# Kernel optimization log

Hardware: AMD Instinct MI355X
Metric: run time of the kernel (lower is better)

The kernel has to match this reference:

```python
import jax, jax.numpy as jnp
import numpy as np
from jax import lax

B, T, F_IN = 8, 512, 229
C1 = 48            # model_size_conv // 16
C3 = 96            # model_size_conv // 8
D_CONV = 768       # model_size_conv
D_LSTM = 768       # model_size_lstm
N_PITCH = 88       # MAX_MIDI - MIN_MIDI + 1
N_STATE = 5
EMB = 2
LSTM_IN = D_CONV + N_PITCH * EMB   # 944
FC_IN = C3 * (F_IN // 4)           # 96 * 57 = 5472
BN_EPS = 1e-5


def setup_inputs() -> dict:
    key = jax.random.key(0)
    ks = iter(jax.random.split(key, 64))
    nrm = lambda shape, s=0.05: jax.random.normal(next(ks), shape, jnp.float32) * s
    uni = lambda shape: jax.random.uniform(next(ks), shape, jnp.float32, 0.5, 1.5)
    inp = {
        'mel': jax.random.normal(next(ks), (B, T, F_IN), jnp.float32),
        'conv1_w': nrm((C1, 1, 3, 3)), 'conv1_b': nrm((C1,)),
        'bn1_g': uni((C1,)), 'bn1_b': nrm((C1,)), 'bn1_m': nrm((C1,), 0.1), 'bn1_v': uni((C1,)),
        'conv2_w': nrm((C1, C1, 3, 3)), 'conv2_b': nrm((C1,)),
        'bn2_g': uni((C1,)), 'bn2_b': nrm((C1,)), 'bn2_m': nrm((C1,), 0.1), 'bn2_v': uni((C1,)),
        'conv3_w': nrm((C3, C1, 3, 3)), 'conv3_b': nrm((C3,)),
        'bn3_g': uni((C3,)), 'bn3_b': nrm((C3,)), 'bn3_m': nrm((C3,), 0.1), 'bn3_v': uni((C3,)),
        'fc_w': nrm((D_CONV, FC_IN)), 'fc_b': nrm((D_CONV,)),
        'wih1': nrm((4 * D_LSTM, LSTM_IN)), 'whh1': nrm((4 * D_LSTM, D_LSTM)),
        'bih1': nrm((4 * D_LSTM,)), 'bhh1': nrm((4 * D_LSTM,)),
        'wih2': nrm((4 * D_LSTM, D_LSTM)), 'whh2': nrm((4 * D_LSTM, D_LSTM)),
        'bih2': nrm((4 * D_LSTM,)), 'bhh2': nrm((4 * D_LSTM,)),
        'post_w': nrm((N_PITCH * N_STATE, D_LSTM)), 'post_b': nrm((N_PITCH * N_STATE,)),
        'emb_w': nrm((N_STATE, EMB), 1.0),
    }
    return inp


def _conv_bn_relu(x, w, b, g, be, m, v):
    # x: NCHW, w: OIHW, padding 'SAME' == padding=1 for 3x3
    y = lax.conv_general_dilated(x, w, (1, 1), 'SAME', dimension_numbers=('NCHW', 'OIHW', 'NCHW'))
    y = y + b[None, :, None, None]
    scale = (g / jnp.sqrt(v + BN_EPS))[None, :, None, None]
    y = (y - m[None, :, None, None]) * scale + be[None, :, None, None]
    return jax.nn.relu(y)


def _maxpool12(x):
    # MaxPool2d((1,2)) on NCHW, floor mode
    return lax.reduce_window(x, -jnp.inf, lax.max, (1, 1, 1, 2), (1, 1, 1, 2), 'VALID')


def _lstm_cell(x, h, c, wih, whh, bih, bhh):
    z = x @ wih.T + h @ whh.T + bih + bhh
    i, f, g, o = jnp.split(z, 4, axis=-1)
    c = jax.nn.sigmoid(f) * c + jax.nn.sigmoid(i) * jnp.tanh(g)
    h = jax.nn.sigmoid(o) * jnp.tanh(c)
    return h, c


def _forward(mel, conv1_w, conv1_b, bn1_g, bn1_b, bn1_m, bn1_v,
             conv2_w, conv2_b, bn2_g, bn2_b, bn2_m, bn2_v,
             conv3_w, conv3_b, bn3_g, bn3_b, bn3_m, bn3_v,
             fc_w, fc_b, wih1, whh1, bih1, bhh1, wih2, whh2, bih2, bhh2,
             post_w, post_b, emb_w):
    b = mel.shape[0]
    # --- ConvStack acoustic model (eval mode: dropout = identity) ---
    x = mel[:, None]                                  # (B,1,T,F)
    x = _conv_bn_relu(x, conv1_w, conv1_b, bn1_g, bn1_b, bn1_m, bn1_v)
    x = _conv_bn_relu(x, conv2_w, conv2_b, bn2_g, bn2_b, bn2_m, bn2_v)
    x = _maxpool12(x)
    x = _conv_bn_relu(x, conv3_w, conv3_b, bn3_g, bn3_b, bn3_m, bn3_v)
    x = _maxpool12(x)                                 # (B,C3,T,F//4)
    x = x.transpose(0, 2, 1, 3).reshape(b, -1, FC_IN) # (B,T,C3*F//4)
    acoustic = x @ fc_w.T + fc_b                      # (B,T,768)

    def step(carry, a_t):
        h1, c1, h2, c2, prev = carry                  # prev: (B,88) int32
        emb = emb_w[prev].reshape(prev.shape[0], N_PITCH * EMB)
        xt = jnp.concatenate([a_t, emb], axis=-1)     # (B,944)
        h1n, c1n = _lstm_cell(xt, h1, c1, wih1, whh1, bih1, bhh1)
        h2n, c2n = _lstm_cell(h1n, h2, c2, wih2, whh2, bih2, bhh2)
        logits = (h2n @ post_w.T + post_b).reshape(-1, N_PITCH, N_STATE)
        nprev = jnp.argmax(logits, axis=-1).astype(jnp.int32)  # argmax(softmax)==argmax(logits)
        return (h1n, c1n, h2n, c2n, nprev), logits

    z = jnp.zeros((b, D_LSTM), mel.dtype)
    prev0 = jnp.zeros((b, N_PITCH), jnp.int32)
    _, logits = lax.scan(step, (z, z, z, z, prev0), acoustic.transpose(1, 0, 2))
    return logits.transpose(1, 0, 2, 3)               # (B,T,88,N_STATE)


def reference(mel, conv1_w, conv1_b, bn1_g, bn1_b, bn1_m, bn1_v,
              conv2_w, conv2_b, bn2_g, bn2_b, bn2_m, bn2_v,
              conv3_w, conv3_b, bn3_g, bn3_b, bn3_m, bn3_v,
              fc_w, fc_b, wih1, whh1, bih1, bhh1, wih2, whh2, bih2, bhh2,
              post_w, post_b, emb_w):
    return _forward(mel, conv1_w, conv1_b, bn1_g, bn1_b, bn1_m, bn1_v,
                    conv2_w, conv2_b, bn2_g, bn2_b, bn2_m, bn2_v,
                    conv3_w, conv3_b, bn3_g, bn3_b, bn3_m, bn3_v,
                    fc_w, fc_b, wih1, whh1, bih1, bhh1, wih2, whh2, bih2, bhh2,
                    post_w, post_b, emb_w)
```

## Files before the change

### kernel.cpp

```cpp
#include <hip/hip_runtime.h>
#include <math.h>

#define WS_C3   0u
#define WS_C2CH 22413312u
#define WS_AC   28104192u
#define WS_A1   0u

__device__ __forceinline__ float sigm(float x){ return 1.0f / (1.0f + expf(-x)); }

__device__ __forceinline__ void cstore(float* p, float v){
  union { float f; unsigned u; } c; c.f = v;
  __hip_atomic_store((unsigned*)p, c.u, __ATOMIC_RELAXED,
                     __HIP_MEMORY_SCOPE_SYSTEM);
}
__device__ __forceinline__ void cload64(const float* p, float& a, float& b){
  unsigned long long u = __hip_atomic_load((const unsigned long long*)p,
                          __ATOMIC_RELAXED, __HIP_MEMORY_SCOPE_SYSTEM);
  union { unsigned long long u; float f[2]; } c; c.u = u;
  a = c.f[0]; b = c.f[1];
}
__device__ __forceinline__ unsigned cloadu(const unsigned* p){
  return __hip_atomic_load(p, __ATOMIC_RELAXED, __HIP_MEMORY_SCOPE_SYSTEM);
}
__device__ __forceinline__ unsigned long long cloadu64(const void* p){
  return __hip_atomic_load((const unsigned long long*)p, __ATOMIC_RELAXED,
                           __HIP_MEMORY_SCOPE_SYSTEM);
}
__device__ __forceinline__ void cstoreu64(void* p, unsigned long long v){
  __hip_atomic_store((unsigned long long*)p, v, __ATOMIC_RELAXED,
                     __HIP_MEMORY_SCOPE_SYSTEM);
}

#define SLOT 16
#define FLG  4112
__device__ __forceinline__ void gbar(unsigned* sy, unsigned bar, int wg){
  __syncthreads();
  const int tid = threadIdx.x;
  if (tid == 0)
    __hip_atomic_store(&sy[SLOT + wg*16], bar, __ATOMIC_RELAXED,
                       __HIP_MEMORY_SCOPE_SYSTEM);
  if (wg == 255){
    if (tid < 64){
      for (;;){
        unsigned m0 = cloadu(&sy[SLOT + (4*tid + 0)*16]);
        unsigned m1 = cloadu(&sy[SLOT + (4*tid + 1)*16]);
        unsigned m2 = cloadu(&sy[SLOT + (4*tid + 2)*16]);
        unsigned m3 = cloadu(&sy[SLOT + (4*tid + 3)*16]);
        unsigned a = m0 < m1 ? m0 : m1;
        unsigned b = m2 < m3 ? m2 : m3;
        unsigned mn = a < b ? a : b;
        if (__all(mn >= bar)) break;
        __builtin_amdgcn_s_sleep(1);
      }
    }
    __syncthreads();
    __hip_atomic_store(&sy[FLG + tid*16], bar, __ATOMIC_RELAXED,
                       __HIP_MEMORY_SCOPE_SYSTEM);
  } else {
    if (tid == 0){
      while (cloadu(&sy[FLG + wg*16]) < bar)
        __builtin_amdgcn_s_sleep(1);
    }
  }
  __syncthreads();
}

__global__ __launch_bounds__(256) void conv2f_k(
    const float* __restrict__ mel, const float* __restrict__ w1,
    const float* __restrict__ b1, const float* __restrict__ g1,
    const float* __restrict__ be1, const float* __restrict__ m1,
    const float* __restrict__ v1,
    const float* __restrict__ w2, const float* __restrict__ b2,
    const float* __restrict__ g2, const float* __restrict__ be2,
    const float* __restrict__ m2, const float* __restrict__ v2,
    float* __restrict__ c2ch, int t0)
{
  __shared__ float act[3*8*240];
  __shared__ float w2s[48*8*12];
  __shared__ float mel5[5*240];
  __shared__ float w1s[48*12];
  __shared__ float sc1[48], sh1[48], sc2[48], sh2[48];
  int tid = threadIdx.x;
  int b = blockIdx.x / 130, lt = blockIdx.x - b*130;
  int t = t0 - 1 + lt;

  int fg = tid % 29, ocg = tid / 29;
  int f0 = fg * 8, oc0 = ocg * 6;

  if (t < 0 || t > 511){
    if (tid < 232){
      for (int o = 0; o < 6; ++o)
        for (int jj = 0; jj < 4; ++jj){
          int fp = fg*4 + jj;
          if (fp < 114)
            c2ch[((b*48 + oc0 + o)*130 + lt)*114 + fp] = 0.f;
        }
    }
    return;
  }

  for (int idx = tid; idx < 5*240; idx += 256){
    int rr = idx / 240, w = idx - rr*240;
    int tt = t + rr - 2, f = w - 2;
    mel5[idx] = (tt >= 0 && tt < 512 && f >= 0 && f < 229)
                ? mel[(b*512 + tt)*229 + f] : 0.f;
  }
  for (int idx = tid; idx < 48*12; idx += 256){
    int c = idx / 12, q = idx - c*12;
    int kh = q >> 2, kw = q & 3;
    w1s[idx] = (kw < 3) ? w1[c*9 + kh*3 + kw] : 0.f;
  }
  if (tid < 48){
    float s1 = g1[tid] / sqrtf(v1[tid] + 1e-5f);
    sc1[tid] = s1; sh1[tid] = be1[tid] + (b1[tid] - m1[tid]) * s1;
    float s2 = g2[tid] / sqrtf(v2[tid] + 1e-5f);
    sc2[tid] = s2; sh2[tid] = be2[tid] + (b2[tid] - m2[tid]) * s2;
  }

  float acc[6][8];
  #pragma unroll
  for (int o = 0; o < 6; ++o)
    #pragma unroll
    for (int j = 0; j < 8; ++j) acc[o][j] = 0.f;

  for (int ch = 0; ch < 6; ++ch){
    int ci0 = ch * 8;
    __syncthreads();
    for (int idx = tid; idx < 3*8*240; idx += 256){
      int rr = idx / 1920;
      int rem = idx - rr*1920;
      int ci = rem / 240, w = rem - ci*240;
      int tt = t + rr - 1, f = w - 1;
      float val = 0.f;
      if (tt >= 0 && tt < 512 && f >= 0 && f < 229){
        int cg = ci0 + ci;
        float a = 0.f;
        #pragma unroll
        for (int dh = 0; dh < 3; ++dh){
          const float* mr = &mel5[(rr + dh)*240 + w];
          a = fmaf(mr[0], w1s[cg*12 + dh*4 + 0], a);
          a = fmaf(mr[1], w1s[cg*12 + dh*4 + 1], a);
          a = fmaf(mr[2], w1s[cg*12 + dh*4 + 2], a);
        }
        a = a * sc1[cg] + sh1[cg];
        val = a > 0.f ? a : 0.f;
      }
      act[idx] = val;
    }
    for (int idx = tid; idx < 48*8*12; idx += 256){
      int oc = idx / 96;
      int rem = idx - oc*96;
      int ci = rem / 12, q = rem - ci*12;
      int kh = q >> 2, kw = q & 3;
      w2s[idx] = (kw < 3) ? w2[(oc*48 + ci0 + ci)*9 + kh*3 + kw] : 0.f;
    }
    __syncthreads();
    if (tid < 232){
      for (int ci = 0; ci < 8; ++ci){
        #pragma unroll
        for (int kh = 0; kh < 3; ++kh){
          const float* ap = &act[(kh*8 + ci)*240 + f0];
          float4 A0 = *(const float4*)(ap);
          float4 A1v = *(const float4*)(ap + 4);
          float4 A2 = *(const float4*)(ap + 8);
          float L[12] = {A0.x,A0.y,A0.z,A0.w,A1v.x,A1v.y,A1v.z,A1v.w,A2.x,A2.y,A2.z,A2.w};
          #pragma unroll
          for (int o = 0; o < 6; ++o){
            float4 wv = *(const float4*)&w2s[((oc0 + o)*8 + ci)*12 + kh*4];
            #pragma unroll
            for (int j = 0; j < 8; ++j)
              acc[o][j] = fmaf(L[j+2], wv.z, fmaf(L[j+1], wv.y, fmaf(L[j], wv.x, acc[o][j])));
          }
        }
      }
    }
  }
  __syncthreads();
  if (tid < 232){
    #pragma unroll
    for (int o = 0; o < 6; ++o){
      int oc = oc0 + o;
      float s = sc2[oc], hs = sh2[oc];
      #pragma unroll
      for (int jj = 0; jj < 4; ++jj){
        int fp = fg*4 + jj;
        if (fp < 114){
          float v0 = acc[o][2*jj] * s + hs;   v0 = v0 > 0.f ? v0 : 0.f;
          float v1 = acc[o][2*jj+1] * s + hs; v1 = v1 > 0.f ? v1 : 0.f;
          c2ch[((b*48 + oc)*130 + lt)*114 + fp] = v0 > v1 ? v0 : v1;
        }
      }
    }
  }
}

__global__ __launch_bounds__(256) void conv3_k(
    const float* __restrict__ c2ch, const float* __restrict__ w3,
    const float* __restrict__ b3, const float* __restrict__ g3,
    const float* __restrict__ be3, const float* __restrict__ m3,
    const float* __restrict__ v3, float* __restrict__ c3p, int t0)
{
  __shared__ float act[3*8*128];
  __shared__ float w3s[96*8*12];
  __shared__ float sc[96], sh[96];
  int tid = threadIdx.x;
  int b = blockIdx.x >> 7, tl = blockIdx.x & 127;
  int t = t0 + tl;
  if (tid < 96){
    float s = g3[tid] / sqrtf(v3[tid] + 1e-5f);
    sc[tid] = s; sh[tid] = be3[tid] + (b3[tid] - m3[tid]) * s;
  }
  int fg = tid % 15, ocg = tid / 15;
  int f0 = fg * 8, oc0 = ocg * 6;
  float acc[6][8];
  #pragma unroll
  for (int o = 0; o < 6; ++o)
    #pragma unroll
    for (int j = 0; j < 8; ++j) acc[o][j] = 0.f;

  for (int ch = 0; ch < 6; ++ch){
    int ci0 = ch * 8;
    __syncthreads();
    for (int idx = tid; idx < 3*8*128; idx += 256){
      int rr = idx >> 10;
      int rem = idx & 1023;
      int ci = rem >> 7, w = rem & 127;
      int lt = tl + rr;
      int f = w - 1;
      float val = 0.f;
      if (f >= 0 && f < 114)
        val = c2ch[((b*48 + ci0 + ci)*130 + lt)*114 + f];
      act[idx] = val;
    }
    for (int idx = tid; idx < 96*8*12; idx += 256){
      int oc = idx / 96;
      int rem = idx - oc*96;
      int ci = rem / 12, q = rem - ci*12;
      int kh = q >> 2, kw = q & 3;
      w3s[idx] = (kw < 3) ? w3[(oc*48 + ci0 + ci)*9 + kh*3 + kw] : 0.f;
    }
    __syncthreads();
    if (tid < 240){
      for (int ci = 0; ci < 8; ++ci){
        #pragma unroll
        for (int kh = 0; kh < 3; ++kh){
          const float* ap = &act[(kh*8 + ci)*128 + f0];
          float4 A0 = *(const float4*)(ap);
          float4 A1v = *(const float4*)(ap + 4);
          float4 A2 = *(const float4*)(ap + 8);
          float L[12] = {A0.x,A0.y,A0.z,A0.w,A1v.x,A1v.y,A1v.z,A1v.w,A2.x,A2.y,A2.z,A2.w};
          #pragma unroll
          for (int o = 0; o < 6; ++o){
            float4 wv = *(const float4*)&w3s[((oc0 + o)*8 + ci)*12 + kh*4];
            #pragma unroll
            for (int j = 0; j < 8; ++j)
              acc[o][j] = fmaf(L[j+2], wv.z, fmaf(L[j+1], wv.y, fmaf(L[j], wv.x, acc[o][j])));
          }
        }
      }
    }
  }
  __syncthreads();
  if (tid < 240){
    #pragma unroll
    for (int o = 0; o < 6; ++o){
      int oc = oc0 + o;
      float s = sc[oc], hs = sh[oc];
      #pragma unroll
      for (int jj = 0; jj < 4; ++jj){
        int fp = fg*4 + jj;
        if (fp < 57){
          float v0 = acc[o][2*jj] * s + hs;   v0 = v0 > 0.f ? v0 : 0.f;
          float v1 = acc[o][2*jj+1] * s + hs; v1 = v1 > 0.f ? v1 : 0.f;
          c3p[((b*96 + oc)*512 + t)*57 + fp] = v0 > v1 ? v0 : v1;
        }
      }
    }
  }
}

__global__ __launch_bounds__(256) void gemm_fc_k(
    const float* __restrict__ c3p, const float* __restrict__ fcw,
    const float* __restrict__ fcb, float* __restrict__ ac)
{
  __shared__ float As[16*132];
  __shared__ float Bs[16*132];
  int tid = threadIdx.x;
  int m0 = blockIdx.x * 128, n0 = blockIdx.y * 128;
  int tm = (tid & 15) * 8, tn = (tid >> 4) * 8;
  float acc[8][8];
  #pragma unroll
  for (int i = 0; i < 8; ++i)
    #pragma unroll
    for (int j = 0; j < 8; ++j) acc[i][j] = 0.f;

  for (int k0 = 0; k0 < 5472; k0 += 16){
    __syncthreads();
    #pragma unroll
    for (int i = 0; i < 8; ++i){
      int idx = i*256 + tid;
      int k = idx & 15, mm = idx >> 4;
      int gk = k0 + k;
      int ci = (gk * 36793) >> 21;
      int f  = gk - ci*57;
      int gm = m0 + mm;
      int bb = gm >> 9, tt = gm & 511;
      As[k*132 + mm] = c3p[((bb*96 + ci)*512 + tt)*57 + f];
      Bs[k*132 + mm] = fcw[(n0 + mm)*5472 + gk];
    }
    __syncthreads();
    #pragma unroll
    for (int k = 0; k < 16; ++k){
      const float* arow = &As[k*132 + tm];
      const float* brow = &Bs[k*132 + tn];
      float4 a0 = *(const float4*)arow, a1 = *(const float4*)(arow + 4);
      float4 b0 = *(const float4*)brow, b1 = *(const float4*)(brow + 4);
      float av[8] = {a0.x,a0.y,a0.z,a0.w,a1.x,a1.y,a1.z,a1.w};
      float bv[8] = {b0.x,b0.y,b0.z,b0.w,b1.x,b1.y,b1.z,b1.w};
      #pragma unroll
      for (int i = 0; i < 8; ++i)
        #pragma unroll
        for (int j = 0; j < 8; ++j)
          acc[i][j] = fmaf(av[i], bv[j], acc[i][j]);
    }
  }
  #pragma unroll
  for (int i = 0; i < 8; ++i){
    int gm = m0 + tm + i;
    #pragma unroll
    for (int j = 0; j < 8; ++j){
      int gn = n0 + tn + j;
      ac[gm*768 + gn] = acc[i][j] + fcb[gn];
    }
  }
}

__global__ __launch_bounds__(256) void gemm_a1_k(
    const float* __restrict__ ac, const float* __restrict__ wih1,
    const float* __restrict__ bih1, const float* __restrict__ bhh1,
    float* __restrict__ A1)
{
  __shared__ float As[16*132];
  __shared__ float Bs[16*132];
  int tid = threadIdx.x;
  int m0 = blockIdx.x * 128, n0 = blockIdx.y * 128;
  int tm = (tid & 15) * 8, tn = (tid >> 4) * 8;
  float acc[8][8];
  #pragma unroll
  for (int i = 0; i < 8; ++i)
    #pragma unroll
    for (int j = 0; j < 8; ++j) acc[i][j] = 0.f;

  for (int k0 = 0; k0 < 768; k0 += 16){
    __syncthreads();
    #pragma unroll
    for (int i = 0; i < 8; ++i){
      int idx = i*256 + tid;
      int k = idx & 15, mm = idx >> 4;
      int gk = k0 + k;
      As[k*132 + mm] = ac[(m0 + mm)*768 + gk];
      Bs[k*132 + mm] = wih1[(n0 + mm)*944 + gk];
    }
    __syncthreads();
    #pragma unroll
    for (int k = 0; k < 16; ++k){
      const float* arow = &As[k*132 + tm];
      const float* brow = &Bs[k*132 + tn];
      float4 a0 = *(const float4*)arow, a1 = *(const float4*)(arow + 4);
      float4 b0 = *(const float4*)brow, b1 = *(const float4*)(brow + 4);
      float av[8] = {a0.x,a0.y,a0.z,a0.w,a1.x,a1.y,a1.z,a1.w};
      float bv[8] = {b0.x,b0.y,b0.z,b0.w,b1.x,b1.y,b1.z,b1.w};
      #pragma unroll
      for (int i = 0; i < 8; ++i)
        #pragma unroll
        for (int j = 0; j < 8; ++j)
          acc[i][j] = fmaf(av[i], bv[j], acc[i][j]);
    }
  }
  #pragma unroll
  for (int i = 0; i < 8; ++i){
    int gm = m0 + tm + i;
    int tt = gm & 511, bb = gm >> 9;
    #pragma unroll
    for (int j = 0; j < 8; ++j){
      int gn = n0 + tn + j;
      A1[tt*24576 + gn*8 + bb] = acc[i][j] + bih1[gn] + bhh1[gn];
    }
  }
}

#define S2 772
__global__ __launch_bounds__(256, 1) void rec_k(
    const float* __restrict__ A1,
    const float* __restrict__ whh1, const float* __restrict__ wih1,
    const float* __restrict__ wih2, const float* __restrict__ whh2,
    const float* __restrict__ bih2, const float* __restrict__ bhh2,
    const float* __restrict__ postw, const float* __restrict__ postb,
    const float* __restrict__ embw,
    float* __restrict__ xbuf, float* __restrict__ hbuf,
    unsigned* __restrict__ slt, unsigned* __restrict__ sy,
    float* __restrict__ out)
{
  const int wg = blockIdx.x, tid = threadIdx.x;
  const int wv = tid >> 6, l = tid & 63;
  __shared__ float xs[8*S2];
  __shared__ float h2s[8*S2];
  __shared__ float cvec[88*5*12];
  __shared__ float zbuf[96];
  __shared__ float red2[160];
  __shared__ unsigned smax[88];

  float wA[12][3];
  float wB[24][3];
  float wC[3][5];
  {
    int Rb = wv*768 + wg*3;
    #pragma unroll
    for (int ki = 0; ki < 12; ++ki){
      int k = l + (ki << 6);
      #pragma unroll
      for (int u = 0; u < 3; ++u)
        wA[ki][u] = whh1[(Rb + u)*768 + k];
    }
    #pragma unroll
    for (int ki = 0; ki < 24; ++ki){
      int k = l + (ki << 6);
      #pragma unroll
      for (int u = 0; u < 3; ++u)
        wB[ki][u] = (k < 768) ? wih2[(Rb + u)*768 + k] : whh2[(Rb + u)*768 + k - 768];
    }
  }
  if (wg < 88){
    #pragma unroll
    for (int kc = 0; kc < 3; ++kc)
      #pragma unroll
      for (int s = 0; s < 5; ++s)
        wC[kc][s] = postw[(wg*5 + s)*768 + tid + (kc << 8)];
  }
  float b2r = 0.f; int fR = 0, fb = 0;
  if (tid < 96){
    int g = tid / 24, rem = tid - g*24;
    int u = rem >> 3; fb = rem & 7;
    fR = g*768 + wg*3 + u;
    b2r = bih2[fR] + bhh2[fR];
  }
  float pbr = (wg < 88 && tid < 40) ? postb[wg*5 + (tid >> 3)] : 0.f;
  float c1r = 0.f, c2r = 0.f;

  for (int idx = tid; idx < 88*5*12; idx += 256){
    int p = idx / 60, rem = idx - p*60;
    int s = rem / 12, r = rem - s*12;
    int g = r / 3, u = r - g*3;
    int row = g*768 + wg*3 + u;
    cvec[idx] = wih1[row*944 + 768 + 2*p]     * embw[s*2]
              + wih1[row*944 + 768 + 2*p + 1] * embw[s*2 + 1];
  }
  for (int idx = tid; idx < 8*S2; idx += 256){ h2s[idx] = 0.f; xs[idx] = 0.f; }
  __syncthreads();

  unsigned bar = 0;

  for (int t = 0; t < 512; ++t){
    float* xn = xbuf + (t & 1) * 6144;
    float* hw = hbuf + (t & 1) * 6144;
    const float* hr = hbuf + ((t ^ 1) & 1) * 6144;

    float a1v = 0.f;
    if (tid < 96) a1v = A1[t*24576 + fR*8 + fb];

    float r0[8], r1[8], r2[8];
    #pragma unroll
    for (int q = 0; q < 8; ++q){ r0[q] = 0.f; r1[q] = 0.f; r2[q] = 0.f; }
    if (t > 0){
      #pragma unroll
      for (int q = 0; q < 4; ++q){
        cload64(hr + (tid      )*8 + 2*q, r0[2*q], r0[2*q+1]);
        cload64(hr + (tid + 256)*8 + 2*q, r1[2*q], r1[2*q+1]);
        cload64(hr + (tid + 512)*8 + 2*q, r2[2*q], r2[2*q+1]);
      }
      if (wg < 88){
        float accL[5][8];
        #pragma unroll
        for (int s = 0; s < 5; ++s)
          #pragma unroll
          for (int j = 0; j < 8; ++j)
            accL[s][j] = fmaf(wC[2][s], r2[j],
                         fmaf(wC[1][s], r1[j], wC[0][s]*r0[j]));
        #pragma unroll
        for (int s = 0; s < 5; ++s)
          #pragma unroll
          for (int j = 0; j < 8; ++j){
            float v = accL[s][j];
            v += __shfl_xor(v, 1);  v += __shfl_xor(v, 2);  v += __shfl_xor(v, 4);
            v += __shfl_xor(v, 8);  v += __shfl_xor(v, 16); v += __shfl_xor(v, 32);
            if (l == 0) red2[(s*8 + j)*4 + wv] = v;
          }
        __syncthreads();
        if (tid < 40){
          float sum = red2[tid*4] + red2[tid*4 + 1] + red2[tid*4 + 2] + red2[tid*4 + 3] + pbr;
          int s = tid >> 3, bb = tid & 7;
          out[bb*225280 + (t-1)*440 + wg*5 + s] = sum;
          zbuf[tid] = sum;
        }
        __syncthreads();
        int bs = 0;
        if (tid < 8){
          float best = zbuf[tid];
          #pragma unroll
          for (int s = 1; s < 5; ++s){
            float v = zbuf[s*8 + tid];
            if (v > best){ best = v; bs = s; }
          }
        }
        if (wv == 0){
          unsigned lo = 0;
          #pragma unroll
          for (int b = 0; b < 8; ++b)
            lo |= (unsigned)(__shfl(bs, b) & 7) << (4*b);
          if (l == 0){
            unsigned long long pv =
                ((unsigned long long)(unsigned)t << 32) | (unsigned long long)lo;
            cstoreu64((unsigned long long*)slt + ((size_t)(t & 1)*88 + wg)*8, pv);
          }
        }
      }
    }

    float acc1[3][8];
    #pragma unroll
    for (int u = 0; u < 3; ++u)
      #pragma unroll
      for (int j = 0; j < 8; ++j) acc1[u][j] = 0.f;
    #pragma unroll
    for (int ki = 0; ki < 12; ++ki){
      int k = l + (ki << 6);
      float x0 = xs[k],        x1 = xs[S2 + k],   x2 = xs[2*S2 + k], x3 = xs[3*S2 + k];
      float x4 = xs[4*S2 + k], x5 = xs[5*S2 + k], x6 = xs[6*S2 + k], x7 = xs[7*S2 + k];
      #pragma unroll
      for (int u = 0; u < 3; ++u){
        float w = wA[ki][u];
        acc1[u][0] = fmaf(w, x0, acc1[u][0]);
        acc1[u][1] = fmaf(w, x1, acc1[u][1]);
        acc1[u][2] = fmaf(w, x2, acc1[u][2]);
        acc1[u][3] = fmaf(w, x3, acc1[u][3]);
        acc1[u][4] = fmaf(w, x4, acc1[u][4]);
        acc1[u][5] = fmaf(w, x5, acc1[u][5]);
        acc1[u][6] = fmaf(w, x6, acc1[u][6]);
        acc1[u][7] = fmaf(w, x7, acc1[u][7]);
      }
    }

    __syncthreads();
    #pragma unroll
    for (int p = 0; p < 8; ++p){
      h2s[p*S2 + tid]       = r0[p];
      h2s[p*S2 + tid + 256] = r1[p];
      h2s[p*S2 + tid + 512] = r2[p];
    }
    #pragma unroll
    for (int u = 0; u < 3; ++u)
      #pragma unroll
      for (int j = 0; j < 8; ++j){
        float s = acc1[u][j];
        s += __shfl_xor(s, 1);  s += __shfl_xor(s, 2);  s += __shfl_xor(s, 4);
        s += __shfl_xor(s, 8);  s += __shfl_xor(s, 16); s += __shfl_xor(s, 32);
        if (l == 0) zbuf[wv*24 + u*8 + j] = s;
      }
    if (wv == 0){
      const unsigned long long* sl =
          (const unsigned long long*)slt + (size_t)(t & 1) * 88 * 8;
      unsigned lo0 = 0, lo1 = 0;
      for (;;){
        unsigned long long v0 = cloadu64(&sl[l*8]);
        unsigned long long v1 = 0xffffffffffffffffull;
        if (l < 24) v1 = cloadu64(&sl[(64 + l)*8]);
        unsigned t0v = (unsigned)(v0 >> 32);
        unsigned t1v = (unsigned)(v1 >> 32);
        unsigned mn = t0v < t1v ? t0v : t1v;
        if (__all(mn >= (unsigned)t)){ lo0 = (unsigned)v0; lo1 = (unsigned)v1; break; }
        __builtin_amdgcn_s_sleep(1);
      }
      smax[l] = lo0;
      if (l < 24) smax[64 + l] = lo1;
    }
    __syncthreads();
    if (tid < 96){
      int g = tid / 24;
      int rowidx = g*3 + ((tid - g*24) >> 3);
      int b = tid & 7;
      float z = zbuf[tid] + a1v;
      for (int p = 0; p < 88; ++p){
        int s = (smax[p] >> (b*4)) & 7;
        z += cvec[(p*5 + s)*12 + rowidx];
      }
      zbuf[tid] = z;
    }
    __syncthreads();
    if (tid < 24){
      float zi = zbuf[tid], zf = zbuf[24 + tid], zg = zbuf[48 + tid], zo = zbuf[72 + tid];
      c1r = sigm(zf)*c1r + sigm(zi)*tanhf(zg);
      float hh = sigm(zo)*tanhf(c1r);
      cstore(&xn[wg*24 + tid], hh);
    }
    ++bar; gbar(sy, bar, wg);

    {
      float sa[12], sb[12];
      #pragma unroll
      for (int i = 0; i < 12; ++i){
        int idx = tid + (i << 8);
        cload64(xn + 2*idx, sa[i], sb[i]);
      }
      float acc[3][8];
      #pragma unroll
      for (int u = 0; u < 3; ++u)
        #pragma unroll
        for (int j = 0; j < 8; ++j) acc[u][j] = 0.f;
      #pragma unroll
      for (int ki = 12; ki < 24; ++ki){
        int k = l + ((ki - 12) << 6);
        float x0 = h2s[k],        x1 = h2s[S2 + k],   x2 = h2s[2*S2 + k], x3 = h2s[3*S2 + k];
        float x4 = h2s[4*S2 + k], x5 = h2s[5*S2 + k], x6 = h2s[6*S2 + k], x7 = h2s[7*S2 + k];
        #pragma unroll
        for (int u = 0; u < 3; ++u){
          float w = wB[ki][u];
          acc[u][0] = fmaf(w, x0, acc[u][0]);
          acc[u][1] = fmaf(w, x1, acc[u][1]);
          acc[u][2] = fmaf(w, x2, acc[u][2]);
          acc[u][3] = fmaf(w, x3, acc[u][3]);
          acc[u][4] = fmaf(w, x4, acc[u][4]);
          acc[u][5] = fmaf(w, x5, acc[u][5]);
          acc[u][6] = fmaf(w, x6, acc[u][6]);
          acc[u][7] = fmaf(w, x7, acc[u][7]);
        }
      }
      #pragma unroll
      for (int i = 0; i < 12; ++i){
        int idx = tid + (i << 8);
        int k = idx >> 2, p = (idx & 3) << 1;
        xs[p*S2 + k]       = sa[i];
        xs[(p + 1)*S2 + k] = sb[i];
      }
      __syncthreads();
      #pragma unroll
      for (int ki = 0; ki < 12; ++ki){
        int k = l + (ki << 6);
        float x0 = xs[k],        x1 = xs[S2 + k],   x2 = xs[2*S2 + k], x3 = xs[3*S2 + k];
        float x4 = xs[4*S2 + k], x5 = xs[5*S2 + k], x6 = xs[6*S2 + k], x7 = xs[7*S2 + k];
        #pragma unroll
        for (int u = 0; u < 3; ++u){
          float w = wB[ki][u];
          acc[u][0] = fmaf(w, x0, acc[u][0]);
          acc[u][1] = fmaf(w, x1, acc[u][1]);
          acc[u][2] = fmaf(w, x2, acc[u][2]);
          acc[u][3] = fmaf(w, x3, acc[u][3]);
          acc[u][4] = fmaf(w, x4, acc[u][4]);
          acc[u][5] = fmaf(w, x5, acc[u][5]);
          acc[u][6] = fmaf(w, x6, acc[u][6]);
          acc[u][7] = fmaf(w, x7, acc[u][7]);
        }
      }
      #pragma unroll
      for (int u = 0; u < 3; ++u)
        #pragma unroll
        for (int j = 0; j < 8; ++j){
          float s = acc[u][j];
          s += __shfl_xor(s, 1);  s += __shfl_xor(s, 2);  s += __shfl_xor(s, 4);
          s += __shfl_xor(s, 8);  s += __shfl_xor(s, 16); s += __shfl_xor(s, 32);
          if (l == 0) zbuf[wv*24 + u*8 + j] = s;
        }
      __syncthreads();
      if (tid < 96)
        zbuf[tid] += b2r;
      __syncthreads();
      if (tid < 24){
        float zi = zbuf[tid], zf = zbuf[24 + tid], zg = zbuf[48 + tid], zo = zbuf[72 + tid];
        c2r = sigm(zf)*c2r + sigm(zi)*tanhf(zg);
        float hh = sigm(zo)*tanhf(c2r);
        cstore(&hw[wg*24 + tid], hh);
      }
      ++bar; gbar(sy, bar, wg);
    }
  }

  if (wg < 88){
    const float* hr = hbuf + 6144;
    float r0[8], r1[8], r2[8];
    #pragma unroll
    for (int q = 0; q < 4; ++q){
      cload64(hr + (tid      )*8 + 2*q, r0[2*q], r0[2*q+1]);
      cload64(hr + (tid + 256)*8 + 2*q, r1[2*q], r1[2*q+1]);
      cload64(hr + (tid + 512)*8 + 2*q, r2[2*q], r2[2*q+1]);
    }
    float accL[5][8];
    #pragma unroll
    for (int s = 0; s < 5; ++s)
      #pragma unroll
      for (int j = 0; j < 8; ++j)
        accL[s][j] = fmaf(wC[2][s], r2[j],
                     fmaf(wC[1][s], r1[j], wC[0][s]*r0[j]));
    #pragma unroll
    for (int s = 0; s < 5; ++s)
      #pragma unroll
      for (int j = 0; j < 8; ++j){
        float v = accL[s][j];
        v += __shfl_xor(v, 1);  v += __shfl_xor(v, 2);  v += __shfl_xor(v, 4);
        v += __shfl_xor(v, 8);  v += __shfl_xor(v, 16); v += __shfl_xor(v, 32);
        if (l == 0) red2[(s*8 + j)*4 + wv] = v;
      }
    __syncthreads();
    if (tid < 40){
      float sum = red2[tid*4] + red2[tid*4 + 1] + red2[tid*4 + 2] + red2[tid*4 + 3] + pbr;
      int s = tid >> 3, bb = tid & 7;
      out[bb*225280 + 511*440 + wg*5 + s] = sum;
    }
  }
}

extern "C" void kernel_launch(void* const* d_in, const int* in_sizes, int n_in,
                              void* d_out, int out_size, void* d_ws, size_t ws_size,
                              hipStream_t stream)
{
  (void)in_sizes; (void)n_in; (void)out_size; (void)ws_size;
  const float* mel  = (const float*)d_in[0];
  const float* w1   = (const float*)d_in[1];
  const float* b1   = (const float*)d_in[2];
  const float* g1   = (const float*)d_in[3];
  const float* be1  = (const float*)d_in[4];
  const float* m1   = (const float*)d_in[5];
  const float* v1   = (const float*)d_in[6];
  const float* w2   = (const float*)d_in[7];
  const float* b2   = (const float*)d_in[8];
  const float* g2   = (const float*)d_in[9];
  const float* be2  = (const float*)d_in[10];
  const float* m2   = (const float*)d_in[11];
  const float* v2   = (const float*)d_in[12];
  const float* w3   = (const float*)d_in[13];
  const float* b3   = (const float*)d_in[14];
  const float* g3   = (const float*)d_in[15];
  const float* be3  = (const float*)d_in[16];
  const float* m3   = (const float*)d_in[17];
  const float* v3   = (const float*)d_in[18];
  const float* fcw  = (const float*)d_in[19];
  const float* fcb  = (const float*)d_in[20];
  const float* wih1 = (const float*)d_in[21];
  const float* whh1 = (const float*)d_in[22];
  const float* bih1 = (const float*)d_in[23];
  const float* bhh1 = (const float*)d_in[24];
  const float* wih2 = (const float*)d_in[25];
  const float* whh2 = (const float*)d_in[26];
  const float* bih2 = (const float*)d_in[27];
  const float* bhh2 = (const float*)d_in[28];
  const float* postw= (const float*)d_in[29];
  const float* postb= (const float*)d_in[30];
  const float* embw = (const float*)d_in[31];

  float* ws    = (float*)d_ws;
  float* c3p   = ws + WS_C3;
  float* c2ch  = ws + WS_C2CH;
  float* ac    = ws + WS_AC;
  float* A1    = ws + WS_A1;
  float* st    = ws + WS_AC;
  float* xbuf  = st;
  float* hbuf  = st + 12288;
  unsigned* slt = (unsigned*)(st + 24576);
  unsigned* sy  = (unsigned*)(st + 27392);
  float* outp  = (float*)d_out;

  for (int c = 0; c < 4; ++c){
    int t0 = c * 128;
    conv2f_k<<<dim3(8*130), dim3(256), 0, stream>>>(
        mel, w1, b1, g1, be1, m1, v1, w2, b2, g2, be2, m2, v2, c2ch, t0);
    conv3_k<<<dim3(8*128), dim3(256), 0, stream>>>(
        c2ch, w3, b3, g3, be3, m3, v3, c3p, t0);
  }
  gemm_fc_k<<<dim3(32, 6), dim3(256), 0, stream>>>(c3p, fcw, fcb, ac);
  gemm_a1_k<<<dim3(32, 24), dim3(256), 0, stream>>>(ac, wih1, bih1, bhh1, A1);

  hipMemsetAsync(st, 0, 35600 * sizeof(float), stream);

  rec_k<<<dim3(256), dim3(256), 0, stream>>>(
      A1, whh1, wih1, wih2, whh2, bih2, bhh2, postw, postb, embw,
      xbuf, hbuf, slt, sy, outp);
}
```

Before: 19.06 ms.

## Overlap output projection and argmax with the grid barrier using tagged h2 slots

Splits the grid barrier into arrive and wait phases. The 88 post-projection workgroups now poll tagged 64-bit h2 values (timestep in the high word) and compute logits and argmax for the current step between arrive and wait, instead of after the next barrier. This moves the projection and argmax off the critical path of the next step's input stage. In exchange it adds a second h2 buffer with tag words, per-element spin polling, and a larger workspace memset.

```diff
diff --git a/kernel.cpp b/kernel.cpp
--- a/kernel.cpp
+++ b/kernel.cpp
@@ -30,15 +30,23 @@
   __hip_atomic_store((unsigned long long*)p, v, __ATOMIC_RELAXED,
                      __HIP_MEMORY_SCOPE_SYSTEM);
 }
+__device__ __forceinline__ float u2f(unsigned u){
+  union { unsigned u; float f; } c; c.u = u; return c.f;
+}
+__device__ __forceinline__ unsigned f2u(float f){
+  union { unsigned u; float f; } c; c.f = f; return c.u;
+}
 
 #define SLOT 16
 #define FLG  4112
-__device__ __forceinline__ void gbar(unsigned* sy, unsigned bar, int wg){
+__device__ __forceinline__ void gbar_arrive(unsigned* sy, unsigned bar, int wg){
   __syncthreads();
-  const int tid = threadIdx.x;
-  if (tid == 0)
+  if (threadIdx.x == 0)
     __hip_atomic_store(&sy[SLOT + wg*16], bar, __ATOMIC_RELAXED,
                        __HIP_MEMORY_SCOPE_SYSTEM);
+}
+__device__ __forceinline__ void gbar_wait(unsigned* sy, unsigned bar, int wg){
+  const int tid = threadIdx.x;
   if (wg == 255){
     if (tid < 64){
       for (;;){
@@ -63,6 +71,10 @@
     }
   }
   __syncthreads();
+}
+__device__ __forceinline__ void gbar(unsigned* sy, unsigned bar, int wg){
+  gbar_arrive(sy, bar, wg);
+  gbar_wait(sy, bar, wg);
 }
 
 __global__ __launch_bounds__(256) void conv2f_k(
@@ -398,6 +410,7 @@
     const float* __restrict__ postw, const float* __restrict__ postb,
     const float* __restrict__ embw,
     float* __restrict__ xbuf, float* __restrict__ hbuf,
+    unsigned long long* __restrict__ hat,
     unsigned* __restrict__ slt, unsigned* __restrict__ sy,
     float* __restrict__ out)
 {
@@ -459,70 +472,25 @@
   __syncthreads();
 
   unsigned bar = 0;
+  float r0[8], r1[8], r2[8];
+  #pragma unroll
+  for (int q = 0; q < 8; ++q){ r0[q] = 0.f; r1[q] = 0.f; r2[q] = 0.f; }
 
   for (int t = 0; t < 512; ++t){
     float* xn = xbuf + (t & 1) * 6144;
     float* hw = hbuf + (t & 1) * 6144;
+    unsigned long long* hwt = hat + (size_t)(t & 1) * 6144;
     const float* hr = hbuf + ((t ^ 1) & 1) * 6144;
 
     float a1v = 0.f;
     if (tid < 96) a1v = A1[t*24576 + fR*8 + fb];
 
-    float r0[8], r1[8], r2[8];
-    #pragma unroll
-    for (int q = 0; q < 8; ++q){ r0[q] = 0.f; r1[q] = 0.f; r2[q] = 0.f; }
-    if (t > 0){
+    if (wg >= 88 && t > 0){
       #pragma unroll
       for (int q = 0; q < 4; ++q){
         cload64(hr + (tid      )*8 + 2*q, r0[2*q], r0[2*q+1]);
         cload64(hr + (tid + 256)*8 + 2*q, r1[2*q], r1[2*q+1]);
         cload64(hr + (tid + 512)*8 + 2*q, r2[2*q], r2[2*q+1]);
-      }
-      if (wg < 88){
-        float accL[5][8];
-        #pragma unroll
-        for (int s = 0; s < 5; ++s)
-          #pragma unroll
-          for (int j = 0; j < 8; ++j)
-            accL[s][j] = fmaf(wC[2][s], r2[j],
-                         fmaf(wC[1][s], r1[j], wC[0][s]*r0[j]));
-        #pragma unroll
-        for (int s = 0; s < 5; ++s)
-          #pragma unroll
-          for (int j = 0; j < 8; ++j){
-            float v = accL[s][j];
-            v += __shfl_xor(v, 1);  v += __shfl_xor(v, 2);  v += __shfl_xor(v, 4);
-            v += __shfl_xor(v, 8);  v += __shfl_xor(v, 16); v += __shfl_xor(v, 32);
-            if (l == 0) red2[(s*8 + j)*4 + wv] = v;
-          }
-        __syncthreads();
-        if (tid < 40){
-          float sum = red2[tid*4] + red2[tid*4 + 1] + red2[tid*4 + 2] + red2[tid*4 + 3] + pbr;
-          int s = tid >> 3, bb = tid & 7;
-          out[bb*225280 + (t-1)*440 + wg*5 + s] = sum;
-          zbuf[tid] = sum;
-        }
-        __syncthreads();
-        int bs = 0;
-        if (tid < 8){
-          float best = zbuf[tid];
-          #pragma unroll
-          for (int s = 1; s < 5; ++s){
-            float v = zbuf[s*8 + tid];
-            if (v > best){ best = v; bs = s; }
-          }
-        }
-        if (wv == 0){
-          unsigned lo = 0;
-          #pragma unroll
-          for (int b = 0; b < 8; ++b)
-            lo |= (unsigned)(__shfl(bs, b) & 7) << (4*b);
-          if (l == 0){
-            unsigned long long pv =
-                ((unsigned long long)(unsigned)t << 32) | (unsigned long long)lo;
-            cstoreu64((unsigned long long*)slt + ((size_t)(t & 1)*88 + wg)*8, pv);
-          }
-        }
       }
     }
 
@@ -552,12 +520,6 @@
 
     __syncthreads();
     #pragma unroll
-    for (int p = 0; p < 8; ++p){
-      h2s[p*S2 + tid]       = r0[p];
-      h2s[p*S2 + tid + 256] = r1[p];
-      h2s[p*S2 + tid + 512] = r2[p];
-    }
-    #pragma unroll
     for (int u = 0; u < 3; ++u)
       #pragma unroll
       for (int j = 0; j < 8; ++j){
@@ -566,6 +528,12 @@
         s += __shfl_xor(s, 8);  s += __shfl_xor(s, 16); s += __shfl_xor(s, 32);
         if (l == 0) zbuf[wv*24 + u*8 + j] = s;
       }
+    #pragma unroll
+    for (int p = 0; p < 8; ++p){
+      h2s[p*S2 + tid]       = r0[p];
+      h2s[p*S2 + tid + 256] = r1[p];
+      h2s[p*S2 + tid + 512] = r2[p];
+    }
     if (wv == 0){
       const unsigned long long* sl =
           (const unsigned long long*)slt + (size_t)(t & 1) * 88 * 8;
@@ -678,42 +646,82 @@
         c2r = sigm(zf)*c2r + sigm(zi)*tanhf(zg);
         float hh = sigm(zo)*tanhf(c2r);
         cstore(&hw[wg*24 + tid], hh);
-      }
-      ++bar; gbar(sy, bar, wg);
-    }
-  }
-
-  if (wg < 88){
-    const float* hr = hbuf + 6144;
-    float r0[8], r1[8], r2[8];
-    #pragma unroll
-    for (int q = 0; q < 4; ++q){
-      cload64(hr + (tid      )*8 + 2*q, r0[2*q], r0[2*q+1]);
-      cload64(hr + (tid + 256)*8 + 2*q, r1[2*q], r1[2*q+1]);
-      cload64(hr + (tid + 512)*8 + 2*q, r2[2*q], r2[2*q+1]);
-    }
-    float accL[5][8];
-    #pragma unroll
-    for (int s = 0; s < 5; ++s)
-      #pragma unroll
-      for (int j = 0; j < 8; ++j)
-        accL[s][j] = fmaf(wC[2][s], r2[j],
-                     fmaf(wC[1][s], r1[j], wC[0][s]*r0[j]));
-    #pragma unroll
-    for (int s = 0; s < 5; ++s)
-      #pragma unroll
-      for (int j = 0; j < 8; ++j){
-        float v = accL[s][j];
-        v += __shfl_xor(v, 1);  v += __shfl_xor(v, 2);  v += __shfl_xor(v, 4);
-        v += __shfl_xor(v, 8);  v += __shfl_xor(v, 16); v += __shfl_xor(v, 32);
-        if (l == 0) red2[(s*8 + j)*4 + wv] = v;
-      }
-    __syncthreads();
-    if (tid < 40){
-      float sum = red2[tid*4] + red2[tid*4 + 1] + red2[tid*4 + 2] + red2[tid*4 + 3] + pbr;
-      int s = tid >> 3, bb = tid & 7;
-      out[bb*225280 + 511*440 + wg*5 + s] = sum;
-    }
+        cstoreu64(&hwt[wg*24 + tid],
+                  ((unsigned long long)(unsigned)(t + 1) << 32)
+                  | (unsigned long long)f2u(hh));
+      }
+    }
+
+    ++bar;
+    gbar_arrive(sy, bar, wg);
+    if (wg < 88){
+      const unsigned tg2 = (unsigned)(t + 1);
+      unsigned long long bv[24];
+      #pragma unroll
+      for (int i = 0; i < 24; ++i)
+        bv[i] = cloadu64(&hwt[(tid + ((i >> 3) << 8))*8 + (i & 7)]);
+      for (;;){
+        bool bad = false;
+        #pragma unroll
+        for (int i = 0; i < 24; ++i)
+          if ((unsigned)(bv[i] >> 32) < tg2){
+            bv[i] = cloadu64(&hwt[(tid + ((i >> 3) << 8))*8 + (i & 7)]); bad = true;
+          }
+        if (!__any(bad)) break;
+        __builtin_amdgcn_s_sleep(1);
+      }
+      #pragma unroll
+      for (int q = 0; q < 8; ++q){
+        r0[q] = u2f((unsigned)bv[q]);
+        r1[q] = u2f((unsigned)bv[8 + q]);
+        r2[q] = u2f((unsigned)bv[16 + q]);
+      }
+      float accL[5][8];
+      #pragma unroll
+      for (int s = 0; s < 5; ++s)
+        #pragma unroll
+        for (int j = 0; j < 8; ++j)
+          accL[s][j] = fmaf(wC[2][s], r2[j],
+                       fmaf(wC[1][s], r1[j], wC[0][s]*r0[j]));
+      #pragma unroll
+      for (int s = 0; s < 5; ++s)
+        #pragma unroll
+        for (int j = 0; j < 8; ++j){
+          float v = accL[s][j];
+          v += __shfl_xor(v, 1);  v += __shfl_xor(v, 2);  v += __shfl_xor(v, 4);
+          v += __shfl_xor(v, 8);  v += __shfl_xor(v, 16); v += __shfl_xor(v, 32);
+          if (l == 0) red2[(s*8 + j)*4 + wv] = v;
+        }
+      __syncthreads();
+      if (tid < 40){
+        float sum = red2[tid*4] + red2[tid*4 + 1] + red2[tid*4 + 2] + red2[tid*4 + 3] + pbr;
+        int s = tid >> 3, bb = tid & 7;
+        out[bb*225280 + t*440 + wg*5 + s] = sum;
+        zbuf[tid] = sum;
+      }
+      __syncthreads();
+      int bs = 0;
+      if (tid < 8){
+        float best = zbuf[tid];
+        #pragma unroll
+        for (int s = 1; s < 5; ++s){
+          float v = zbuf[s*8 + tid];
+          if (v > best){ best = v; bs = s; }
+        }
+      }
+      if (wv == 0){
+        unsigned lo = 0;
+        #pragma unroll
+        for (int b = 0; b < 8; ++b)
+          lo |= (unsigned)(__shfl(bs, b) & 7) << (4*b);
+        if (l == 0){
+          unsigned long long pv =
+              ((unsigned long long)(unsigned)(t + 1) << 32) | (unsigned long long)lo;
+          cstoreu64((unsigned long long*)slt + ((size_t)((t + 1) & 1)*88 + wg)*8, pv);
+        }
+      }
+    }
+    gbar_wait(sy, bar, wg);
   }
 }
 
@@ -763,8 +771,9 @@
   float* st    = ws + WS_AC;
   float* xbuf  = st;
   float* hbuf  = st + 12288;
-  unsigned* slt = (unsigned*)(st + 24576);
-  unsigned* sy  = (unsigned*)(st + 27392);
+  unsigned long long* hat = (unsigned long long*)(st + 24576);
+  unsigned* slt = (unsigned*)(st + 49152);
+  unsigned* sy  = (unsigned*)(st + 51968);
   float* outp  = (float*)d_out;
 
   for (int c = 0; c < 4; ++c){
@@ -777,9 +786,9 @@
   gemm_fc_k<<<dim3(32, 6), dim3(256), 0, stream>>>(c3p, fcw, fcb, ac);
   gemm_a1_k<<<dim3(32, 24), dim3(256), 0, stream>>>(ac, wih1, bih1, bhh1, A1);
 
-  hipMemsetAsync(st, 0, 35600 * sizeof(float), stream);
+  hipMemsetAsync(st, 0, 60176 * sizeof(float), stream);
 
   rec_k<<<dim3(256), dim3(256), 0, stream>>>(
       A1, whh1, wih1, wih2, whh2, bih2, bhh2, postw, postb, embw,
-      xbuf, hbuf, slt, sy, outp);
-}
+      xbuf, hbuf, hat, slt, sy, outp);
+}
```

Result: slower. 19.96 ms (+4.7%).

## Fuse conv/GEMM front-end with recurrent LSTM into one persistent kernel

Applied to the files above, without the earlier changes.

Merges the conv2, conv3, FC GEMM and input-projection GEMM stages into a single persistent kernel alongside the LSTM recurrence. Blocks 256-511 compute the front-end in 128-timestep chunks, separated by software grid barriers, and publish a ready flag per chunk. Blocks 0-255 run the recurrence and wait on that flag at each chunk boundary. The intent is to overlap the front-end of later chunks with the serial recurrence on earlier ones and to remove launch gaps. It relies on all 512 blocks being co-resident at 2 blocks per CU. Front-end work now runs on half the grid and uses relaxed atomic loads and stores, which may slow those stages.

```diff
diff --git a/kernel.cpp b/kernel.cpp
--- a/kernel.cpp
+++ b/kernel.cpp
@@ -1,10 +1,13 @@
 #include <hip/hip_runtime.h>
 #include <math.h>
 
-#define WS_C3   0u
-#define WS_C2CH 22413312u
-#define WS_AC   28104192u
-#define WS_A1   0u
+#define OF_C2CH 0u
+#define OF_C3P  5690880u
+#define OF_AC   11294208u
+#define OF_A1   14439936u
+#define OF_ST   27022848u
+#define OF_PSY  27058448u
+#define OF_RDY  27066656u
 
 __device__ __forceinline__ float sigm(float x){ return 1.0f / (1.0f + expf(-x)); }
 
@@ -12,6 +15,11 @@
   union { float f; unsigned u; } c; c.f = v;
   __hip_atomic_store((unsigned*)p, c.u, __ATOMIC_RELAXED,
                      __HIP_MEMORY_SCOPE_SYSTEM);
+}
+__device__ __forceinline__ float cloadf(const float* p){
+  unsigned u = __hip_atomic_load((const unsigned*)p, __ATOMIC_RELAXED,
+                                 __HIP_MEMORY_SCOPE_SYSTEM);
+  union { unsigned u; float f; } c; c.u = u; return c.f;
 }
 __device__ __forceinline__ void cload64(const float* p, float& a, float& b){
   unsigned long long u = __hip_atomic_load((const unsigned long long*)p,
@@ -33,13 +41,13 @@
 
 #define SLOT 16
 #define FLG  4112
-__device__ __forceinline__ void gbar(unsigned* sy, unsigned bar, int wg){
+__device__ __forceinline__ void gbar(unsigned* sy, unsigned bar, int id){
   __syncthreads();
   const int tid = threadIdx.x;
   if (tid == 0)
-    __hip_atomic_store(&sy[SLOT + wg*16], bar, __ATOMIC_RELAXED,
+    __hip_atomic_store(&sy[SLOT + id*16], bar, __ATOMIC_RELAXED,
                        __HIP_MEMORY_SCOPE_SYSTEM);
-  if (wg == 255){
+  if (id == 255){
     if (tid < 64){
       for (;;){
         unsigned m0 = cloadu(&sy[SLOT + (4*tid + 0)*16]);
@@ -58,30 +66,28 @@
                        __HIP_MEMORY_SCOPE_SYSTEM);
   } else {
     if (tid == 0){
-      while (cloadu(&sy[FLG + wg*16]) < bar)
+      while (cloadu(&sy[FLG + id*16]) < bar)
         __builtin_amdgcn_s_sleep(1);
     }
   }
   __syncthreads();
 }
 
-__global__ __launch_bounds__(256) void conv2f_k(
-    const float* __restrict__ mel, const float* __restrict__ w1,
-    const float* __restrict__ b1, const float* __restrict__ g1,
-    const float* __restrict__ be1, const float* __restrict__ m1,
-    const float* __restrict__ v1,
-    const float* __restrict__ w2, const float* __restrict__ b2,
-    const float* __restrict__ g2, const float* __restrict__ be2,
-    const float* __restrict__ m2, const float* __restrict__ v2,
-    float* __restrict__ c2ch, int t0)
+
+__device__ void conv2f_body(float* SH, int vb, int t0,
+    const float* mel, const float* w1, const float* b1, const float* g1,
+    const float* be1, const float* m1, const float* v1,
+    const float* w2, const float* b2, const float* g2, const float* be2,
+    const float* m2, const float* v2, float* c2ch)
 {
-  __shared__ float act[3*8*240];
-  __shared__ float w2s[48*8*12];
-  __shared__ float mel5[5*240];
-  __shared__ float w1s[48*12];
-  __shared__ float sc1[48], sh1[48], sc2[48], sh2[48];
+  float* act  = SH;
+  float* w2s  = SH + 5760;
+  float* mel5 = SH + 10368;
+  float* w1s  = SH + 11568;
+  float* sc1  = SH + 12144; float* sh1 = SH + 12192;
+  float* sc2  = SH + 12240; float* sh2 = SH + 12288;
   int tid = threadIdx.x;
-  int b = blockIdx.x / 130, lt = blockIdx.x - b*130;
+  int b = vb / 130, lt = vb - b*130;
   int t = t0 - 1 + lt;
 
   int fg = tid % 29, ocg = tid / 29;
@@ -93,11 +99,12 @@
         for (int jj = 0; jj < 4; ++jj){
           int fp = fg*4 + jj;
           if (fp < 114)
-            c2ch[((b*48 + oc0 + o)*130 + lt)*114 + fp] = 0.f;
+            cstore(&c2ch[((b*48 + oc0 + o)*130 + lt)*114 + fp], 0.f);
         }
     }
     return;
   }
+  __syncthreads();
 
   for (int idx = tid; idx < 5*240; idx += 256){
     int rr = idx / 240, w = idx - rr*240;
@@ -187,25 +194,23 @@
         if (fp < 114){
           float v0 = acc[o][2*jj] * s + hs;   v0 = v0 > 0.f ? v0 : 0.f;
           float v1 = acc[o][2*jj+1] * s + hs; v1 = v1 > 0.f ? v1 : 0.f;
-          c2ch[((b*48 + oc)*130 + lt)*114 + fp] = v0 > v1 ? v0 : v1;
-        }
-      }
-    }
-  }
-}
-
-__global__ __launch_bounds__(256) void conv3_k(
-    const float* __restrict__ c2ch, const float* __restrict__ w3,
-    const float* __restrict__ b3, const float* __restrict__ g3,
-    const float* __restrict__ be3, const float* __restrict__ m3,
-    const float* __restrict__ v3, float* __restrict__ c3p, int t0)
+          cstore(&c2ch[((b*48 + oc)*130 + lt)*114 + fp], v0 > v1 ? v0 : v1);
+        }
+      }
+    }
+  }
+}
+
+__device__ void conv3_body(float* SH, int vb, int t0,
+    const float* c2ch, const float* w3, const float* b3, const float* g3,
+    const float* be3, const float* m3, const float* v3, float* c3p)
 {
-  __shared__ float act[3*8*128];
-  __shared__ float w3s[96*8*12];
-  __shared__ float sc[96], sh[96];
+  float* act = SH;
+  float* w3s = SH + 3072;
+  float* sc  = SH + 12288; float* sh = SH + 12384;
   int tid = threadIdx.x;
-  int b = blockIdx.x >> 7, tl = blockIdx.x & 127;
-  int t = t0 + tl;
+  int b = vb >> 7, tl = vb & 127;
+  __syncthreads();
   if (tid < 96){
     float s = g3[tid] / sqrtf(v3[tid] + 1e-5f);
     sc[tid] = s; sh[tid] = be3[tid] + (b3[tid] - m3[tid]) * s;
@@ -229,7 +234,7 @@
       int f = w - 1;
       float val = 0.f;
       if (f >= 0 && f < 114)
-        val = c2ch[((b*48 + ci0 + ci)*130 + lt)*114 + f];
+        val = cloadf(&c2ch[((b*48 + ci0 + ci)*130 + lt)*114 + f]);
       act[idx] = val;
     }
     for (int idx = tid; idx < 96*8*12; idx += 256){
@@ -272,21 +277,21 @@
         if (fp < 57){
           float v0 = acc[o][2*jj] * s + hs;   v0 = v0 > 0.f ? v0 : 0.f;
           float v1 = acc[o][2*jj+1] * s + hs; v1 = v1 > 0.f ? v1 : 0.f;
-          c3p[((b*96 + oc)*512 + t)*57 + fp] = v0 > v1 ? v0 : v1;
-        }
-      }
-    }
-  }
-}
-
-__global__ __launch_bounds__(256) void gemm_fc_k(
-    const float* __restrict__ c3p, const float* __restrict__ fcw,
-    const float* __restrict__ fcb, float* __restrict__ ac)
+          cstore(&c3p[((b*96 + oc)*128 + tl)*57 + fp], v0 > v1 ? v0 : v1);
+        }
+      }
+    }
+  }
+}
+
+__device__ void gemmfc_body(float* SH, int vb, int c,
+    const float* c3p, const float* fcw, const float* fcb, float* ac)
 {
-  __shared__ float As[16*132];
-  __shared__ float Bs[16*132];
+  float* As = SH;
+  float* Bs = SH + 2112;
   int tid = threadIdx.x;
-  int m0 = blockIdx.x * 128, n0 = blockIdx.y * 128;
+  int bb = vb & 7, by = vb >> 3;
+  int m0 = (bb*4 + c) * 128, n0 = by * 128;
   int tm = (tid & 15) * 8, tn = (tid >> 4) * 8;
   float acc[8][8];
   #pragma unroll
@@ -304,8 +309,8 @@
       int ci = (gk * 36793) >> 21;
       int f  = gk - ci*57;
       int gm = m0 + mm;
-      int bb = gm >> 9, tt = gm & 511;
-      As[k*132 + mm] = c3p[((bb*96 + ci)*512 + tt)*57 + f];
+      int bb2 = gm >> 9, tt = gm & 511;
+      As[k*132 + mm] = cloadf(&c3p[((bb2*96 + ci)*128 + (tt & 127))*57 + f]);
       Bs[k*132 + mm] = fcw[(n0 + mm)*5472 + gk];
     }
     __syncthreads();
@@ -324,26 +329,27 @@
           acc[i][j] = fmaf(av[i], bv[j], acc[i][j]);
     }
   }
+  __syncthreads();
   #pragma unroll
   for (int i = 0; i < 8; ++i){
     int gm = m0 + tm + i;
     #pragma unroll
     for (int j = 0; j < 8; ++j){
       int gn = n0 + tn + j;
-      ac[gm*768 + gn] = acc[i][j] + fcb[gn];
-    }
-  }
-}
-
-__global__ __launch_bounds__(256) void gemm_a1_k(
-    const float* __restrict__ ac, const float* __restrict__ wih1,
-    const float* __restrict__ bih1, const float* __restrict__ bhh1,
-    float* __restrict__ A1)
+      cstore(&ac[gm*768 + gn], acc[i][j] + fcb[gn]);
+    }
+  }
+}
+
+__device__ void gemma1_body(float* SH, int vb, int c,
+    const float* ac, const float* wih1, const float* bih1,
+    const float* bhh1, float* A1)
 {
-  __shared__ float As[16*132];
-  __shared__ float Bs[16*132];
+  float* As = SH;
+  float* Bs = SH + 2112;
   int tid = threadIdx.x;
-  int m0 = blockIdx.x * 128, n0 = blockIdx.y * 128;
+  int bb = vb & 7, by = vb >> 3;
+  int m0 = (bb*4 + c) * 128, n0 = by * 128;
   int tm = (tid & 15) * 8, tn = (tid >> 4) * 8;
   float acc[8][8];
   #pragma unroll
@@ -358,7 +364,7 @@
       int idx = i*256 + tid;
       int k = idx & 15, mm = idx >> 4;
       int gk = k0 + k;
-      As[k*132 + mm] = ac[(m0 + mm)*768 + gk];
+      As[k*132 + mm] = cloadf(&ac[(m0 + mm)*768 + gk]);
       Bs[k*132 + mm] = wih1[(n0 + mm)*944 + gk];
     }
     __syncthreads();
@@ -377,38 +383,81 @@
           acc[i][j] = fmaf(av[i], bv[j], acc[i][j]);
     }
   }
+  __syncthreads();
   #pragma unroll
   for (int i = 0; i < 8; ++i){
     int gm = m0 + tm + i;
-    int tt = gm & 511, bb = gm >> 9;
+    int tt = gm & 511, bb2 = gm >> 9;
     #pragma unroll
     for (int j = 0; j < 8; ++j){
       int gn = n0 + tn + j;
-      A1[tt*24576 + gn*8 + bb] = acc[i][j] + bih1[gn] + bhh1[gn];
+      cstore(&A1[tt*24576 + gn*8 + bb2], acc[i][j] + bih1[gn] + bhh1[gn]);
     }
   }
 }
 
 #define S2 772
-__global__ __launch_bounds__(256, 1) void rec_k(
-    const float* __restrict__ A1,
-    const float* __restrict__ whh1, const float* __restrict__ wih1,
+__global__ __launch_bounds__(256, 2) void fat_k(
+    const float* __restrict__ mel,
+    const float* __restrict__ w1, const float* __restrict__ b1,
+    const float* __restrict__ g1, const float* __restrict__ be1,
+    const float* __restrict__ m1, const float* __restrict__ v1,
+    const float* __restrict__ w2, const float* __restrict__ b2,
+    const float* __restrict__ g2, const float* __restrict__ be2,
+    const float* __restrict__ m2, const float* __restrict__ v2,
+    const float* __restrict__ w3, const float* __restrict__ b3,
+    const float* __restrict__ g3, const float* __restrict__ be3,
+    const float* __restrict__ m3, const float* __restrict__ v3,
+    const float* __restrict__ fcw, const float* __restrict__ fcb,
+    const float* __restrict__ wih1, const float* __restrict__ whh1,
+    const float* __restrict__ bih1, const float* __restrict__ bhh1,
     const float* __restrict__ wih2, const float* __restrict__ whh2,
     const float* __restrict__ bih2, const float* __restrict__ bhh2,
     const float* __restrict__ postw, const float* __restrict__ postb,
     const float* __restrict__ embw,
+    float* __restrict__ c2ch, float* __restrict__ c3p,
+    float* __restrict__ ac, float* __restrict__ A1,
     float* __restrict__ xbuf, float* __restrict__ hbuf,
     unsigned* __restrict__ slt, unsigned* __restrict__ sy,
+    unsigned* __restrict__ psy, unsigned* __restrict__ rdy,
     float* __restrict__ out)
 {
-  const int wg = blockIdx.x, tid = threadIdx.x;
+  __shared__ float SH[17976];
+  const int wid = blockIdx.x, tid = threadIdx.x;
+
+  if (wid >= 256){
+    const int pid = wid - 256;
+    unsigned pb = 0;
+    for (int c = 0; c < 4; ++c){
+      int t0 = c * 128;
+      for (int vb = pid; vb < 8*130; vb += 256)
+        conv2f_body(SH, vb, t0, mel, w1, b1, g1, be1, m1, v1,
+                    w2, b2, g2, be2, m2, v2, c2ch);
+      ++pb; gbar(psy, pb, pid);
+      for (int vb = pid; vb < 8*128; vb += 256)
+        conv3_body(SH, vb, t0, c2ch, w3, b3, g3, be3, m3, v3, c3p);
+      ++pb; gbar(psy, pb, pid);
+      for (int vb = pid; vb < 48; vb += 256)
+        gemmfc_body(SH, vb, c, c3p, fcw, fcb, ac);
+      ++pb; gbar(psy, pb, pid);
+      for (int vb = pid; vb < 192; vb += 256)
+        gemma1_body(SH, vb, c, ac, wih1, bih1, bhh1, A1);
+      ++pb; gbar(psy, pb, pid);
+      if (pid == 255 && tid == 0)
+        __hip_atomic_store(&rdy[c], 1u, __ATOMIC_RELAXED,
+                           __HIP_MEMORY_SCOPE_SYSTEM);
+    }
+    return;
+  }
+
+  const int wg = wid;
   const int wv = tid >> 6, l = tid & 63;
-  __shared__ float xs[8*S2];
-  __shared__ float h2s[8*S2];
-  __shared__ float cvec[88*5*12];
-  __shared__ float zbuf[96];
-  __shared__ float red2[160];
-  __shared__ unsigned smax[88];
+  float* xs   = SH;
+  float* h2s  = SH + 6176;
+  float* cvec = SH + 12352;
+  float* zbuf = SH + 17632;
+  float* red2 = SH + 17728;
+  unsigned* smax = (unsigned*)(SH + 17888);
 
   float wA[12][3];
   float wB[24][3];
@@ -461,12 +510,22 @@
   unsigned bar = 0;
 
   for (int t = 0; t < 512; ++t){
+    if ((t & 127) == 0){
+      if (tid == 0){
+        const int c = t >> 7;
+        while (__hip_atomic_load(&rdy[c], __ATOMIC_RELAXED,
+                                 __HIP_MEMORY_SCOPE_SYSTEM) == 0)
+          __builtin_amdgcn_s_sleep(1);
+      }
+      __syncthreads();
+    }
+
     float* xn = xbuf + (t & 1) * 6144;
     float* hw = hbuf + (t & 1) * 6144;
     const float* hr = hbuf + ((t ^ 1) & 1) * 6144;
 
     float a1v = 0.f;
-    if (tid < 96) a1v = A1[t*24576 + fR*8 + fb];
+    if (tid < 96) a1v = cloadf(&A1[t*24576 + fR*8 + fb]);
 
     float r0[8], r1[8], r2[8];
     #pragma unroll
@@ -756,30 +815,25 @@
   const float* embw = (const float*)d_in[31];
 
   float* ws    = (float*)d_ws;
-  float* c3p   = ws + WS_C3;
-  float* c2ch  = ws + WS_C2CH;
-  float* ac    = ws + WS_AC;
-  float* A1    = ws + WS_A1;
-  float* st    = ws + WS_AC;
+  float* c2ch  = ws + OF_C2CH;
+  float* c3p   = ws + OF_C3P;
+  float* ac    = ws + OF_AC;
+  float* A1    = ws + OF_A1;
+  float* st    = ws + OF_ST;
   float* xbuf  = st;
   float* hbuf  = st + 12288;
   unsigned* slt = (unsigned*)(st + 24576);
   unsigned* sy  = (unsigned*)(st + 27392);
+  unsigned* psy = (unsigned*)(ws + OF_PSY);
+  unsigned* rdy = (unsigned*)(ws + OF_RDY);
   float* outp  = (float*)d_out;
 
-  for (int c = 0; c < 4; ++c){
-    int t0 = c * 128;
-    conv2f_k<<<dim3(8*130), dim3(256), 0, stream>>>(
-        mel, w1, b1, g1, be1, m1, v1, w2, b2, g2, be2, m2, v2, c2ch, t0);
-    conv3_k<<<dim3(8*128), dim3(256), 0, stream>>>(
-        c2ch, w3, b3, g3, be3, m3, v3, c3p, t0);
-  }
-  gemm_fc_k<<<dim3(32, 6), dim3(256), 0, stream>>>(c3p, fcw, fcb, ac);
-  gemm_a1_k<<<dim3(32, 24), dim3(256), 0, stream>>>(ac, wih1, bih1, bhh1, A1);
-
-  hipMemsetAsync(st, 0, 35600 * sizeof(float), stream);
-
-  rec_k<<<dim3(256), dim3(256), 0, stream>>>(
-      A1, whh1, wih1, wih2, whh2, bih2, bhh2, postw, postb, embw,
-      xbuf, hbuf, slt, sy, outp);
-}
+  hipMemsetAsync(ws + OF_ST, 0, (35600 + 8208 + 16) * sizeof(float), stream);
+
+  fat_k<<<dim3(512), dim3(256), 0, stream>>>(
+      mel, w1, b1, g1, be1, m1, v1, w2, b2, g2, be2, m2, v2,
+      w3, b3, g3, be3, m3, v3, fcw, fcb,
+      wih1, whh1, bih1, bhh1, wih2, whh2, bih2, bhh2,
+      postw, postb, embw,
+      c2ch, c3p, ac, A1, xbuf, hbuf, slt, sy, psy, rdy, outp);
+}
```

New measurement: 35.62 ms. 86.9% more time.
